# Kernel tuning notes

Hardware: AMD Instinct MI355X
Metric: run time of the kernel (lower is better)

Reference implementation:

```python
import jax, jax.numpy as jnp
import numpy as np

D_MODEL = 256
D_INNER = 512      # expand(2) * d_model
D_STATE = 16
DT_RANK = 16       # ceil(256/16)
D_CONV = 4
DEPTH = 2


def _silu(x):
    return x * jax.nn.sigmoid(x)


def _selective_scan(u, dt, A, B, C, D):
    # u,dt: [b,l,d]; A: [d,n]; B,C: [b,l,n]; D: [d]
    dA = jnp.einsum('bld,dn->bldn', dt, A)
    dBu = jnp.einsum('bld,bld,bln->bldn', dt, u, B)
    # torch: F.pad(dA[:,1:], last-l-dim one zero).flip(1).cumsum(1).exp().flip(1)
    dA_shift = jnp.concatenate([dA[:, 1:], jnp.zeros_like(dA[:, :1])], axis=1)
    dAc = jnp.exp(jnp.cumsum(dA_shift[:, ::-1], axis=1)[:, ::-1])
    x = jnp.cumsum(dBu * dAc, axis=1) / (dAc + 1e-12)
    y = jnp.einsum('bldn,bln->bld', x, C)
    return y + u * D


def _block(x, p):
    # x: [b,l,d_model]
    in_w, conv_w, conv_b, xproj_w, dt_w, dt_b, A_log, Dp, out_w = p
    xr = jnp.einsum('bld,ed->ble', x, in_w)           # [b,l,2*d_inner]
    xx, res = jnp.split(xr, 2, axis=-1)
    # causal depthwise conv1d (padding d_conv-1 then truncate == left-pad)
    xc = jax.lax.conv_general_dilated(
        xx.transpose(0, 2, 1), conv_w, window_strides=(1,),
        padding=[(D_CONV - 1, 0)], feature_group_count=D_INNER,
        dimension_numbers=('NCH', 'OIH', 'NCH')) + conv_b[None, :, None]
    xx = _silu(xc.transpose(0, 2, 1))                 # [b,l,d_inner]
    x_dbl = jnp.einsum('bld,ed->ble', xx, xproj_w)
    delta = x_dbl[..., :DT_RANK]
    B = x_dbl[..., DT_RANK:DT_RANK + D_STATE]
    C = x_dbl[..., DT_RANK + D_STATE:]
    delta = jax.nn.softplus(jnp.einsum('blr,dr->bld', delta, dt_w) + dt_b)
    A = -jnp.exp(A_log)
    y = _selective_scan(xx, delta, A, B, C, Dp)
    y = y * _silu(res)
    return jnp.einsum('bld,od->blo', y, out_w)


def _model1(x, params):
    for i in range(DEPTH):
        x = _block(x, tuple(q[i] for q in params))
    return x


def setup_inputs() -> dict:
    key = jax.random.key(0)
    ks = jax.random.split(key, 8)

    def nrm(k, shape, scale):
        return (jax.random.normal(k, shape) * scale).astype(jnp.float32)

    x0 = jax.random.normal(ks[0], (4, D_MODEL, 256, 256), jnp.float32)
    in_w = nrm(ks[1], (DEPTH, 2 * D_INNER, D_MODEL), 0.02)
    conv_w = nrm(ks[2], (DEPTH, D_INNER, 1, D_CONV), 0.1)
    conv_b = jnp.zeros((DEPTH, D_INNER), jnp.float32)
    xproj_w = nrm(ks[3], (DEPTH, DT_RANK + 2 * D_STATE, D_INNER), 0.02)
    dt_w = nrm(ks[4], (DEPTH, D_INNER, DT_RANK), 0.05)
    dt_b = jnp.full((DEPTH, D_INNER), -4.0, jnp.float32)  # small deltas for stability
    A_log = jnp.tile(jnp.log(jnp.arange(1, D_STATE + 1, dtype=jnp.float32))[None, None, :],
                     (DEPTH, D_INNER, 1))
    Dp = jnp.ones((DEPTH, D_INNER), jnp.float32)
    out_w = nrm(ks[5], (DEPTH, D_MODEL, D_INNER), 0.02)
    return dict(x0=x0, in_w=in_w, conv_w=conv_w, conv_b=conv_b, xproj_w=xproj_w,
                dt_w=dt_w, dt_b=dt_b, A_log=A_log, Dp=Dp, out_w=out_w)


def reference(x0, in_w, conv_w, conv_b, xproj_w, dt_w, dt_b, A_log, Dp, out_w):
    params = (in_w, conv_w, conv_b, xproj_w, dt_w, dt_b, A_log, Dp, out_w)
    # h-axis: pool over w, mamba over length h (weights shared with w pass)
    x_h = x0.mean(axis=3)                                        # [b,c,h]
    xm_h = _model1(x_h.transpose(0, 2, 1), params)               # [b,h,c]
    xm_h = xm_h.transpose(0, 2, 1)[..., None] * x0               # [b,c,h,w]
    # w-axis: pool over h of gated map, mamba over length w
    x_w = xm_h.mean(axis=2)                                      # [b,c,w]
    xm_w = _model1(x_w.transpose(0, 2, 1), params)               # [b,w,c]
    return xm_w.transpose(0, 2, 1)[:, :, None, :] * x0           # [b,c,h,w]
```

## Files before the change

kernel.cpp:

```cpp
#include <hip/hip_runtime.h>
#include <math.h>

#define BSZ 4
#define DM 256
#define LL 256
#define DI 512
#define NBL (BSZ * LL)

__device__ __forceinline__ float fast_rcp(float x) { return __builtin_amdgcn_rcpf(x); }
__device__ __forceinline__ float fast_sig(float x) { return fast_rcp(1.0f + __expf(-x)); }

__device__ __forceinline__ void unswz(int j, int& b, int& i) {
    b = (j & 7) >> 1;
    i = ((j >> 3) << 1) | (j & 1);
}

__global__ __launch_bounds__(256) void k_meanw_prep(const float* __restrict__ x0,
                                                    const float* __restrict__ in_w1,
                                                    const float* __restrict__ out_w0,
                                                    float* __restrict__ S0,
                                                    float* __restrict__ Wf) {
    __shared__ float smem[1664];
    int bl = blockIdx.x;
    int tid = threadIdx.x;
    if (bl < 1024) {
        int b, i; unswz(bl, b, i);
        int rowblk = (b << 8) | i;
        int wv = tid >> 6, lane = tid & 63;
        const float4* x4 = (const float4*)x0;
        int rbase = rowblk * 256 + wv * 64;
        for (int i0 = 0; i0 < 64; i0 += 8) {
            float s[8];
#pragma unroll
            for (int j = 0; j < 8; ++j) {
                float4 v = x4[(size_t)(rbase + i0 + j) * 64 + lane];
                s[j] = (v.x + v.y) + (v.z + v.w);
            }
#pragma unroll
            for (int j = 0; j < 8; ++j) {
#pragma unroll
                for (int m = 32; m >= 1; m >>= 1) s[j] += __shfl_xor(s[j], m);
            }
            if (lane == 0) {
#pragma unroll
                for (int j = 0; j < 8; ++j) {
                    int rr = rbase + i0 + j;
                    int bb = rr >> 16, d = (rr >> 8) & 255, h = rr & 255;
                    S0[((size_t)(bb * LL) + h) * DM + d] = s[j] * (1.0f / 256.0f);
                }
            }
        }
    } else {
        float* As = smem;
        float* Bs = smem + 576;
        int t = bl - 1024;
        int e0 = (t >> 4) * 32, k0c = (t & 15) * 32;
        int tx = tid & 15, ty = tid >> 4;
        float acc00 = 0.f, acc01 = 0.f, acc10 = 0.f, acc11 = 0.f;
        for (int dm0 = 0; dm0 < 256; dm0 += 16) {
            float4 v;
            if (tid < 128) {
                int r = tid >> 2, q = tid & 3;
                v = *(const float4*)(in_w1 + (size_t)(e0 + r) * 256 + dm0 + 4 * q);
            } else {
                int idx = tid - 128;
                int r = idx >> 3, q = idx & 7;
                v = *(const float4*)(out_w0 + (size_t)(dm0 + r) * 512 + k0c + 4 * q);
            }
            __syncthreads();
            if (tid < 128) {
                int r = tid >> 2, q = tid & 3;
                As[(4 * q + 0) * 36 + r] = v.x;
                As[(4 * q + 1) * 36 + r] = v.y;
                As[(4 * q + 2) * 36 + r] = v.z;
                As[(4 * q + 3) * 36 + r] = v.w;
            } else {
                int idx = tid - 128;
                int r = idx >> 3, q = idx & 7;
                Bs[r * 36 + 4 * q + 0] = v.x;
                Bs[r * 36 + 4 * q + 1] = v.y;
                Bs[r * 36 + 4 * q + 2] = v.z;
                Bs[r * 36 + 4 * q + 3] = v.w;
            }
            __syncthreads();
#pragma unroll
            for (int kk = 0; kk < 16; ++kk) {
                float2 a = *(const float2*)(As + kk * 36 + 2 * ty);
                float2 b2 = *(const float2*)(Bs + kk * 36 + 2 * tx);
                acc00 = fmaf(a.x, b2.x, acc00);
                acc01 = fmaf(a.x, b2.y, acc01);
                acc10 = fmaf(a.y, b2.x, acc10);
                acc11 = fmaf(a.y, b2.y, acc11);
            }
        }
        float* c0 = Wf + (size_t)(e0 + 2 * ty) * 512 + k0c + 2 * tx;
        c0[0] = acc00; c0[1] = acc01;
        c0[512] = acc10; c0[513] = acc11;
    }
}

__global__ __launch_bounds__(256) void k_gemm_nt64(const float* __restrict__ A,
                                                   const float* __restrict__ Bw,
                                                   float* __restrict__ C) {
    __shared__ float As[16][68];
    __shared__ float Bs[16][68];
    int tid = threadIdx.x;
    int b, i; unswz(blockIdx.x, b, i);
    int m0 = b * 256 + (i >> 4) * 64;
    int n0 = (i & 15) * 64;
    int tx = tid & 15, ty = tid >> 4;
    int r = tid >> 2, kq = (tid & 3) * 4;

    const float* pa = A + (size_t)(m0 + r) * 256 + kq;
    const float* pb = Bw + (size_t)(n0 + r) * 256 + kq;
    float4 ra = *(const float4*)pa;
    float4 rb = *(const float4*)pb;

    float acc[4][4];
#pragma unroll
    for (int ii = 0; ii < 4; ++ii)
#pragma unroll
        for (int jj = 0; jj < 4; ++jj) acc[ii][jj] = 0.0f;

    for (int k0 = 0; k0 < 256; k0 += 16) {
        __syncthreads();
        As[kq + 0][r] = ra.x; As[kq + 1][r] = ra.y; As[kq + 2][r] = ra.z; As[kq + 3][r] = ra.w;
        Bs[kq + 0][r] = rb.x; Bs[kq + 1][r] = rb.y; Bs[kq + 2][r] = rb.z; Bs[kq + 3][r] = rb.w;
        __syncthreads();
        if (k0 + 16 < 256) {
            ra = *(const float4*)(pa + k0 + 16);
            rb = *(const float4*)(pb + k0 + 16);
        }
#pragma unroll
        for (int kk = 0; kk < 16; ++kk) {
            float4 a4 = *(const float4*)(&As[kk][ty * 4]);
            float4 b4 = *(const float4*)(&Bs[kk][tx * 4]);
            float aa[4] = {a4.x, a4.y, a4.z, a4.w};
            float bb[4] = {b4.x, b4.y, b4.z, b4.w};
#pragma unroll
            for (int ii = 0; ii < 4; ++ii)
#pragma unroll
                for (int jj = 0; jj < 4; ++jj)
                    acc[ii][jj] = fmaf(aa[ii], bb[jj], acc[ii][jj]);
        }
    }
#pragma unroll
    for (int ii = 0; ii < 4; ++ii) {
        float4 o;
        o.x = acc[ii][0]; o.y = acc[ii][1]; o.z = acc[ii][2]; o.w = acc[ii][3];
        *(float4*)(C + (size_t)(m0 + ty * 4 + ii) * 1024 + n0 + tx * 4) = o;
    }
}

__global__ __launch_bounds__(256) void k_gemm_tn64(const float* __restrict__ At,
                                                   const float* __restrict__ Bw,
                                                   float* __restrict__ C) {
    __shared__ float As[16][68];
    __shared__ float Bs[16][68];
    int tid = threadIdx.x;
    int b, i; unswz(blockIdx.x, b, i);
    int l0 = (i >> 4) * 64;
    int n0 = (i & 15) * 64;
    int m0 = b * 256 + l0;
    int tx = tid & 15, ty = tid >> 4;
    int rkk = tid >> 4, mq = (tid & 15) * 4;
    int rn = tid >> 2, dq = (tid & 3) * 4;

    const float* pa = At + ((size_t)(b * 512) + rkk) * 256 + l0 + mq;
    const float* pb = Bw + (size_t)(n0 + rn) * 512 + dq;
    float4 ra = *(const float4*)pa;
    float4 rb = *(const float4*)pb;

    float acc[4][4];
#pragma unroll
    for (int ii = 0; ii < 4; ++ii)
#pragma unroll
        for (int jj = 0; jj < 4; ++jj) acc[ii][jj] = 0.0f;

    for (int d0 = 0; d0 < 512; d0 += 16) {
        __syncthreads();
        *(float4*)(&As[rkk][mq]) = ra;
        Bs[dq + 0][rn] = rb.x; Bs[dq + 1][rn] = rb.y; Bs[dq + 2][rn] = rb.z; Bs[dq + 3][rn] = rb.w;
        __syncthreads();
        if (d0 + 16 < 512) {
            ra = *(const float4*)(pa + (size_t)(d0 + 16) * 256);
            rb = *(const float4*)(pb + d0 + 16);
        }
#pragma unroll
        for (int kk = 0; kk < 16; ++kk) {
            float4 a4 = *(const float4*)(&As[kk][ty * 4]);
            float4 b4 = *(const float4*)(&Bs[kk][tx * 4]);
            float aa[4] = {a4.x, a4.y, a4.z, a4.w};
            float bb[4] = {b4.x, b4.y, b4.z, b4.w};
#pragma unroll
            for (int ii = 0; ii < 4; ++ii)
#pragma unroll
                for (int jj = 0; jj < 4; ++jj)
                    acc[ii][jj] = fmaf(aa[ii], bb[jj], acc[ii][jj]);
        }
    }
#pragma unroll
    for (int ii = 0; ii < 4; ++ii) {
        float4 o;
        o.x = acc[ii][0]; o.y = acc[ii][1]; o.z = acc[ii][2]; o.w = acc[ii][3];
        *(float4*)(C + (size_t)(m0 + ty * 4 + ii) * 1024 + n0 + tx * 4) = o;
    }
}

__global__ __launch_bounds__(256) void k_gemm_tn32(const float* __restrict__ At,
                                                   const float* __restrict__ B,
                                                   float* __restrict__ C) {
    __shared__ float As[16 * 36];
    __shared__ float Bs[16 * 36];
    int tid = threadIdx.x;
    int tx = tid & 15, ty = tid >> 4;
    int b, i; unswz(blockIdx.x, b, i);
    int l0 = (i >> 3) * 32;
    int n0 = (i & 7) * 32;
    int m0 = b * 256 + l0;

    float acc00 = 0.f, acc01 = 0.f, acc10 = 0.f, acc11 = 0.f;
    for (int d0 = 0; d0 < 512; d0 += 16) {
        float4 v;
        if (tid < 128) {
            int r = tid >> 3, q = tid & 7;
            v = *(const float4*)(At + ((size_t)(b * 512 + d0 + r)) * 256 + l0 + 4 * q);
        } else {
            int idx = tid - 128;
            int nr = idx >> 2, q = idx & 3;
            v = *(const float4*)(B + (size_t)(n0 + nr) * 512 + d0 + 4 * q);
        }
        __syncthreads();
        if (tid < 128) {
            int r = tid >> 3, q = tid & 7;
            *(float4*)(As + r * 36 + 4 * q) = v;
        } else {
            int idx = tid - 128;
            int nr = idx >> 2, q = idx & 3;
            Bs[(4 * q + 0) * 36 + nr] = v.x;
            Bs[(4 * q + 1) * 36 + nr] = v.y;
            Bs[(4 * q + 2) * 36 + nr] = v.z;
            Bs[(4 * q + 3) * 36 + nr] = v.w;
        }
        __syncthreads();
#pragma unroll
        for (int kk = 0; kk < 16; ++kk) {
            float2 a = *(const float2*)(As + kk * 36 + 2 * ty);
            float2 bb = *(const float2*)(Bs + kk * 36 + 2 * tx);
            acc00 = fmaf(a.x, bb.x, acc00);
            acc01 = fmaf(a.x, bb.y, acc01);
            acc10 = fmaf(a.y, bb.x, acc10);
            acc11 = fmaf(a.y, bb.y, acc11);
        }
    }
    float2 o0; o0.x = acc00; o0.y = acc01;
    float2 o1; o1.x = acc10; o1.y = acc11;
    *(float2*)(C + (size_t)(m0 + 2 * ty + 0) * 256 + n0 + 2 * tx) = o0;
    *(float2*)(C + (size_t)(m0 + 2 * ty + 1) * 256 + n0 + 2 * tx) = o1;
}

__global__ __launch_bounds__(256) void k_mid(const float* __restrict__ xz,
                                             const float* __restrict__ cw,
                                             const float* __restrict__ cb,
                                             const float* __restrict__ xpw,
                                             float* __restrict__ xx,
                                             float* __restrict__ xdbl) {
    __shared__ float xs[DI];
    __shared__ float pr[256];
    int tid = threadIdx.x;
    int b = (blockIdx.x & 7) >> 1;
    int ib = ((blockIdx.x >> 3) << 1) | (blockIdx.x & 1);

    for (int k = 0; k < 4; ++k) {
        int l = ib + 64 * k;
        int bl = (b << 8) | l;
        __syncthreads();
#pragma unroll
        for (int c = 0; c < 2; ++c) {
            int d = tid + 256 * c;
            float4 w4 = *(const float4*)(cw + d * 4);
            float acc = cb[d];
#pragma unroll
            for (int kk = 0; kk < 4; ++kk) {
                int ls = l + kk - 3;
                float v = (ls >= 0) ? xz[((size_t)(b * LL + ls)) * 1024 + d] : 0.0f;
                acc = fmaf(((const float*)&w4)[kk], v, acc);
            }
            float v = acc * fast_sig(acc);
            xs[d] = v;
            xx[(size_t)bl * DI + d] = v;
        }
        __syncthreads();

        int e = tid >> 2, c2 = tid & 3;
        float a = 0.0f;
        if (e < 48) {
            const float4* xv4 = (const float4*)(xs + c2 * 128);
            const float4* wv4 = (const float4*)(xpw + (size_t)e * DI + c2 * 128);
#pragma unroll 8
            for (int q = 0; q < 32; ++q) {
                float4 x4 = xv4[q], p4 = wv4[q];
                a = fmaf(x4.x, p4.x, a);
                a = fmaf(x4.y, p4.y, a);
                a = fmaf(x4.z, p4.z, a);
                a = fmaf(x4.w, p4.w, a);
            }
        }
        pr[tid] = a;
        __syncthreads();
        if (tid < 48)
            xdbl[(size_t)bl * 48 + tid] = pr[4 * tid] + pr[4 * tid + 1] + pr[4 * tid + 2] + pr[4 * tid + 3];
    }
}

__global__ __launch_bounds__(256) void k_scan(const float* __restrict__ xx,
                                              const float* __restrict__ xdbl,
                                              const float* __restrict__ xz,
                                              const float* __restrict__ Alog,
                                              const float* __restrict__ Dp,
                                              const float* __restrict__ dtw,
                                              const float* __restrict__ dtb,
                                              float* __restrict__ ygT) {
    __shared__ float yred[4][LL];
    __shared__ float us[LL];
    int tid = threadIdx.x;
    int lane = tid & 63, w = tid >> 6;
    int b = (blockIdx.x & 7) >> 1;
    int ib = ((blockIdx.x >> 3) << 1) | (blockIdx.x & 1);
    int l0 = lane * 4;

    for (int kq = 0; kq < 4; ++kq) {
        int d = ib + 128 * kq;
        int seq = b * DI + d;
        __syncthreads();

        const float* xd0 = xdbl + ((size_t)(b * LL) + l0) * 48;
        const float* wr = dtw + d * 16;
        float4 w0 = *(const float4*)(wr + 0);
        float4 w1 = *(const float4*)(wr + 4);
        float4 w2 = *(const float4*)(wr + 8);
        float4 w3 = *(const float4*)(wr + 12);
        float bias = dtb[d];

        float dt[4], u[4], dtu[4], P[4];
#pragma unroll
        for (int i = 0; i < 4; ++i) {
            const float* xr = xd0 + i * 48;
            float4 a0 = *(const float4*)(xr + 0);
            float4 a1 = *(const float4*)(xr + 4);
            float4 a2 = *(const float4*)(xr + 8);
            float4 a3 = *(const float4*)(xr + 12);
            float acc = bias;
            acc = fmaf(a0.x, w0.x, acc); acc = fmaf(a0.y, w0.y, acc);
            acc = fmaf(a0.z, w0.z, acc); acc = fmaf(a0.w, w0.w, acc);
            acc = fmaf(a1.x, w1.x, acc); acc = fmaf(a1.y, w1.y, acc);
            acc = fmaf(a1.z, w1.z, acc); acc = fmaf(a1.w, w1.w, acc);
            acc = fmaf(a2.x, w2.x, acc); acc = fmaf(a2.y, w2.y, acc);
            acc = fmaf(a2.z, w2.z, acc); acc = fmaf(a2.w, w2.w, acc);
            acc = fmaf(a3.x, w3.x, acc); acc = fmaf(a3.y, w3.y, acc);
            acc = fmaf(a3.z, w3.z, acc); acc = fmaf(a3.w, w3.w, acc);
            dt[i] = (acc > 20.0f) ? acc : __logf(1.0f + __expf(acc));
            u[i] = xx[((size_t)(b * LL) + l0 + i) * DI + d];
            dtu[i] = dt[i] * u[i];
        }

        P[0] = dt[0]; P[1] = P[0] + dt[1]; P[2] = P[1] + dt[2]; P[3] = P[2] + dt[3];
        float s = P[3];
#pragma unroll
        for (int off = 1; off < 64; off <<= 1) {
            float t = __shfl_up(s, off);
            if (lane >= off) s += t;
        }
        float base = s - P[3];
        float dt_end = __shfl(s, 63);
        float Dtc[4];
#pragma unroll
        for (int i = 0; i < 4; ++i) Dtc[i] = P[i] + base;

        if (w == 0) {
#pragma unroll
            for (int i = 0; i < 4; ++i) us[l0 + i] = u[i];
        }

        float4 Al = *(const float4*)(Alog + d * 16 + 4 * w);
        float A[4] = {-__expf(Al.x), -__expf(Al.y), -__expf(Al.z), -__expf(Al.w)};
        float Bv[4][4], Cv[4][4];
#pragma unroll
        for (int i = 0; i < 4; ++i) {
            float4 bq = *(const float4*)(xd0 + i * 48 + 16 + 4 * w);
            float4 cq = *(const float4*)(xd0 + i * 48 + 32 + 4 * w);
            Bv[i][0] = bq.x; Bv[i][1] = bq.y; Bv[i][2] = bq.z; Bv[i][3] = bq.w;
            Cv[i][0] = cq.x; Cv[i][1] = cq.y; Cv[i][2] = cq.z; Cv[i][3] = cq.w;
        }

        float y[4] = {0.f, 0.f, 0.f, 0.f};
#pragma unroll
        for (int c = 0; c < 4; ++c) {
            float Ac = A[c];
            float dAc[4], t[4];
#pragma unroll
            for (int i = 0; i < 4; ++i) {
                dAc[i] = __expf(Ac * (dt_end - Dtc[i]));
                t[i] = dtu[i] * Bv[i][c] * dAc[i];
            }
            float p0 = t[0], p1 = p0 + t[1], p2 = p1 + t[2], p3 = p2 + t[3];
            float ss = p3;
#pragma unroll
            for (int off = 1; off < 64; off <<= 1) {
                float tt = __shfl_up(ss, off);
                if (lane >= off) ss += tt;
            }
            float baseT = ss - p3;
            y[0] = fmaf((p0 + baseT) * fast_rcp(dAc[0] + 1e-12f), Cv[0][c], y[0]);
            y[1] = fmaf((p1 + baseT) * fast_rcp(dAc[1] + 1e-12f), Cv[1][c], y[1]);
            y[2] = fmaf((p2 + baseT) * fast_rcp(dAc[2] + 1e-12f), Cv[2][c], y[2]);
            y[3] = fmaf((p3 + baseT) * fast_rcp(dAc[3] + 1e-12f), Cv[3][c], y[3]);
        }
#pragma unroll
        for (int i = 0; i < 4; ++i) yred[w][l0 + i] = y[i];
        __syncthreads();

        int l = tid;
        float ysum = yred[0][l] + yred[1][l] + yred[2][l] + yred[3][l];
        float yv = fmaf(us[l], Dp[d], ysum);
        float res = xz[((size_t)(b * LL) + l) * 1024 + DI + d];
        ygT[(size_t)seq * LL + l] = yv * res * fast_sig(res);
    }
}

__global__ __launch_bounds__(256) void k_fuse_mean_h(const float* __restrict__ m,
                                                     const float* __restrict__ x0,
                                                     float* __restrict__ xw) {
    int b, d; unswz(blockIdx.x, b, d);
    int bd = (b << 8) | d;
    int w = threadIdx.x;
    __shared__ float ms[LL];
    ms[w] = m[((size_t)(b * LL) + w) * DM + d];
    __syncthreads();
    const float* xrow = x0 + (size_t)bd * 65536;
    float a0 = 0.0f, a1 = 0.0f, a2 = 0.0f, a3 = 0.0f;
    for (int h = 0; h < 256; h += 8) {
        float xv[8];
#pragma unroll
        for (int j = 0; j < 8; ++j) xv[j] = xrow[(size_t)(h + j) * 256 + w];
        a0 = fmaf(ms[h + 0], xv[0], a0);
        a1 = fmaf(ms[h + 1], xv[1], a1);
        a2 = fmaf(ms[h + 2], xv[2], a2);
        a3 = fmaf(ms[h + 3], xv[3], a3);
        a0 = fmaf(ms[h + 4], xv[4], a0);
        a1 = fmaf(ms[h + 5], xv[5], a1);
        a2 = fmaf(ms[h + 6], xv[6], a2);
        a3 = fmaf(ms[h + 7], xv[7], a3);
    }
    float acc = (a0 + a1) + (a2 + a3);
    xw[((size_t)(b * LL) + w) * DM + d] = acc * (1.0f / 256.0f);
}

__global__ __launch_bounds__(256) void k_final(const float* __restrict__ mw,
                                               const float* __restrict__ x0,
                                               float* __restrict__ out) {
    __shared__ float ms[LL];
    int b, d; unswz(blockIdx.x, b, d);
    int bd = (b << 8) | d;
    int tid = threadIdx.x;
    ms[tid] = mw[((size_t)(b * LL) + tid) * DM + d];
    __syncthreads();

    int w4 = tid & 63;
    int hq = tid >> 6;
    float4 mv = *(const float4*)(ms + (w4 << 2));
    const float4* xin = (const float4*)(x0 + (size_t)bd * 65536);
    float4* oout = (float4*)(out + (size_t)bd * 65536);
#pragma unroll 4
    for (int hi = 0; hi < 64; ++hi) {
        int h = hi * 4 + hq;
        size_t idx = (size_t)h * 64 + w4;
        float4 xv = xin[idx];
        float4 o;
        o.x = mv.x * xv.x;
        o.y = mv.y * xv.y;
        o.z = mv.z * xv.z;
        o.w = mv.w * xv.w;
        oout[idx] = o;
    }
}

extern "C" void kernel_launch(void* const* d_in, const int* in_sizes, int n_in,
                              void* d_out, int out_size, void* d_ws, size_t ws_size,
                              hipStream_t stream) {
    const float* x0      = (const float*)d_in[0];
    const float* in_w    = (const float*)d_in[1];
    const float* conv_w  = (const float*)d_in[2];
    const float* conv_b  = (const float*)d_in[3];
    const float* xproj_w = (const float*)d_in[4];
    const float* dt_w    = (const float*)d_in[5];
    const float* dt_b    = (const float*)d_in[6];
    const float* A_log   = (const float*)d_in[7];
    const float* Dp      = (const float*)d_in[8];
    const float* out_w   = (const float*)d_in[9];
    float* out = (float*)d_out;

    float* S0   = (float*)d_ws;
    float* Sout = S0 + 262144;
    float* Wf   = Sout + 262144;
    float* xz   = Wf + 524288;
    float* xx   = xz + 1048576;
    float* xdbl = xx + 524288;
    float* ygT  = xdbl + 49152;

    const float* out_w1 = out_w + 131072;

    auto run_model = [&](const float* inb, float* outb) {
        k_gemm_nt64<<<256, 256, 0, stream>>>(inb, in_w, xz);
        k_mid<<<256, 256, 0, stream>>>(xz, conv_w, conv_b, xproj_w, xx, xdbl);
        k_scan<<<512, 256, 0, stream>>>(xx, xdbl, xz, A_log, Dp, dt_w, dt_b, ygT);
        k_gemm_tn64<<<256, 256, 0, stream>>>(ygT, Wf, xz);
        k_mid<<<256, 256, 0, stream>>>(xz, conv_w + 2048, conv_b + 512,
                                       xproj_w + 24576, xx, xdbl);
        k_scan<<<512, 256, 0, stream>>>(xx, xdbl, xz, A_log + 8192, Dp + 512,
                                        dt_w + 8192, dt_b + 512, ygT);
        k_gemm_tn32<<<256, 256, 0, stream>>>(ygT, out_w1, outb);
    };

    k_meanw_prep<<<1536, 256, 0, stream>>>(x0, in_w + 262144, out_w, S0, Wf);
    run_model(S0, Sout);
    k_fuse_mean_h<<<NBL, 256, 0, stream>>>(Sout, x0, S0);
    run_model(S0, Sout);
    k_final<<<NBL, 256, 0, stream>>>(Sout, x0, out);
}
```

Before: 479.0 us.

## Fuse final out-projection GEMM into the mean-h and final gating kernels

Removes the standalone out-projection GEMM kernel. Each (b,d) block of the downstream gating kernels now computes its own column of the out-projection, a dot over 512 inner channels for all 256 positions, before doing the x0 pass. This saves two launches and the round trip of the intermediate Sout buffer. In exchange, each block reads a 512x256 slab of ygT, which makes the ygT traffic redundant across the 256 d-blocks that share a batch, though much of it should hit in cache.

```diff
diff --git a/kernel.cpp b/kernel.cpp
--- a/kernel.cpp
+++ b/kernel.cpp
@@ -205,58 +205,6 @@
         o.x = acc[ii][0]; o.y = acc[ii][1]; o.z = acc[ii][2]; o.w = acc[ii][3];
         *(float4*)(C + (size_t)(m0 + ty * 4 + ii) * 1024 + n0 + tx * 4) = o;
     }
-}
-
-__global__ __launch_bounds__(256) void k_gemm_tn32(const float* __restrict__ At,
-                                                   const float* __restrict__ B,
-                                                   float* __restrict__ C) {
-    __shared__ float As[16 * 36];
-    __shared__ float Bs[16 * 36];
-    int tid = threadIdx.x;
-    int tx = tid & 15, ty = tid >> 4;
-    int b, i; unswz(blockIdx.x, b, i);
-    int l0 = (i >> 3) * 32;
-    int n0 = (i & 7) * 32;
-    int m0 = b * 256 + l0;
-
-    float acc00 = 0.f, acc01 = 0.f, acc10 = 0.f, acc11 = 0.f;
-    for (int d0 = 0; d0 < 512; d0 += 16) {
-        float4 v;
-        if (tid < 128) {
-            int r = tid >> 3, q = tid & 7;
-            v = *(const float4*)(At + ((size_t)(b * 512 + d0 + r)) * 256 + l0 + 4 * q);
-        } else {
-            int idx = tid - 128;
-            int nr = idx >> 2, q = idx & 3;
-            v = *(const float4*)(B + (size_t)(n0 + nr) * 512 + d0 + 4 * q);
-        }
-        __syncthreads();
-        if (tid < 128) {
-            int r = tid >> 3, q = tid & 7;
-            *(float4*)(As + r * 36 + 4 * q) = v;
-        } else {
-            int idx = tid - 128;
-            int nr = idx >> 2, q = idx & 3;
-            Bs[(4 * q + 0) * 36 + nr] = v.x;
-            Bs[(4 * q + 1) * 36 + nr] = v.y;
-            Bs[(4 * q + 2) * 36 + nr] = v.z;
-            Bs[(4 * q + 3) * 36 + nr] = v.w;
-        }
-        __syncthreads();
-#pragma unroll
-        for (int kk = 0; kk < 16; ++kk) {
-            float2 a = *(const float2*)(As + kk * 36 + 2 * ty);
-            float2 bb = *(const float2*)(Bs + kk * 36 + 2 * tx);
-            acc00 = fmaf(a.x, bb.x, acc00);
-            acc01 = fmaf(a.x, bb.y, acc01);
-            acc10 = fmaf(a.y, bb.x, acc10);
-            acc11 = fmaf(a.y, bb.y, acc11);
-        }
-    }
-    float2 o0; o0.x = acc00; o0.y = acc01;
-    float2 o1; o1.x = acc10; o1.y = acc11;
-    *(float2*)(C + (size_t)(m0 + 2 * ty + 0) * 256 + n0 + 2 * tx) = o0;
-    *(float2*)(C + (size_t)(m0 + 2 * ty + 1) * 256 + n0 + 2 * tx) = o1;
 }
 
 __global__ __launch_bounds__(256) void k_mid(const float* __restrict__ xz,
@@ -428,15 +376,46 @@
     }
 }
 
-__global__ __launch_bounds__(256) void k_fuse_mean_h(const float* __restrict__ m,
-                                                     const float* __restrict__ x0,
-                                                     float* __restrict__ xw) {
+__device__ __forceinline__ void outproj_col(const float* __restrict__ ygT,
+                                            const float* __restrict__ w1row,
+                                            int b, int tid,
+                                            float* ws, float* ms) {
+    ws[tid] = w1row[tid];
+    ws[tid + 256] = w1row[tid + 256];
+    __syncthreads();
+    const float* yb = ygT + (size_t)(b * 512) * 256 + tid;
+    float a0 = 0.f, a1 = 0.f, a2 = 0.f, a3 = 0.f;
+#pragma unroll 2
+    for (int dd = 0; dd < 512; dd += 8) {
+        float v0 = yb[(dd + 0) * 256], v1 = yb[(dd + 1) * 256];
+        float v2 = yb[(dd + 2) * 256], v3 = yb[(dd + 3) * 256];
+        float v4 = yb[(dd + 4) * 256], v5 = yb[(dd + 5) * 256];
+        float v6 = yb[(dd + 6) * 256], v7 = yb[(dd + 7) * 256];
+        a0 = fmaf(v0, ws[dd + 0], a0);
+        a1 = fmaf(v1, ws[dd + 1], a1);
+        a2 = fmaf(v2, ws[dd + 2], a2);
+        a3 = fmaf(v3, ws[dd + 3], a3);
+        a0 = fmaf(v4, ws[dd + 4], a0);
+        a1 = fmaf(v5, ws[dd + 5], a1);
+        a2 = fmaf(v6, ws[dd + 6], a2);
+        a3 = fmaf(v7, ws[dd + 7], a3);
+    }
+    ms[tid] = (a0 + a1) + (a2 + a3);
+    __syncthreads();
+}
+
+__global__ __launch_bounds__(256) void k_outproj_fuse_mean_h(const float* __restrict__ ygT,
+                                                             const float* __restrict__ w1,
+                                                             const float* __restrict__ x0,
+                                                             float* __restrict__ xw) {
+    __shared__ float ws[512];
+    __shared__ float ms[LL];
     int b, d; unswz(blockIdx.x, b, d);
     int bd = (b << 8) | d;
-    int w = threadIdx.x;
-    __shared__ float ms[LL];
-    ms[w] = m[((size_t)(b * LL) + w) * DM + d];
-    __syncthreads();
+    int tid = threadIdx.x;
+    outproj_col(ygT, w1 + (size_t)d * 512, b, tid, ws, ms);
+
+    int w = tid;
     const float* xrow = x0 + (size_t)bd * 65536;
     float a0 = 0.0f, a1 = 0.0f, a2 = 0.0f, a3 = 0.0f;
     for (int h = 0; h < 256; h += 8) {
@@ -456,15 +435,16 @@
     xw[((size_t)(b * LL) + w) * DM + d] = acc * (1.0f / 256.0f);
 }
 
-__global__ __launch_bounds__(256) void k_final(const float* __restrict__ mw,
-                                               const float* __restrict__ x0,
-                                               float* __restrict__ out) {
+__global__ __launch_bounds__(256) void k_outproj_final(const float* __restrict__ ygT,
+                                                       const float* __restrict__ w1,
+                                                       const float* __restrict__ x0,
+                                                       float* __restrict__ out) {
+    __shared__ float ws[512];
     __shared__ float ms[LL];
     int b, d; unswz(blockIdx.x, b, d);
     int bd = (b << 8) | d;
     int tid = threadIdx.x;
-    ms[tid] = mw[((size_t)(b * LL) + tid) * DM + d];
-    __syncthreads();
+    outproj_col(ygT, w1 + (size_t)d * 512, b, tid, ws, ms);
 
     int w4 = tid & 63;
     int hq = tid >> 6;
@@ -501,8 +481,7 @@
     float* out = (float*)d_out;
 
     float* S0   = (float*)d_ws;
-    float* Sout = S0 + 262144;
-    float* Wf   = Sout + 262144;
+    float* Wf   = S0 + 262144;
     float* xz   = Wf + 524288;
     float* xx   = xz + 1048576;
     float* xdbl = xx + 524288;
@@ -510,7 +489,7 @@
 
     const float* out_w1 = out_w + 131072;
 
-    auto run_model = [&](const float* inb, float* outb) {
+    auto run_model_core = [&](const float* inb) {
         k_gemm_nt64<<<256, 256, 0, stream>>>(inb, in_w, xz);
         k_mid<<<256, 256, 0, stream>>>(xz, conv_w, conv_b, xproj_w, xx, xdbl);
         k_scan<<<512, 256, 0, stream>>>(xx, xdbl, xz, A_log, Dp, dt_w, dt_b, ygT);
@@ -519,12 +498,11 @@
                                        xproj_w + 24576, xx, xdbl);
         k_scan<<<512, 256, 0, stream>>>(xx, xdbl, xz, A_log + 8192, Dp + 512,
                                         dt_w + 8192, dt_b + 512, ygT);
-        k_gemm_tn32<<<256, 256, 0, stream>>>(ygT, out_w1, outb);
     };
 
     k_meanw_prep<<<1536, 256, 0, stream>>>(x0, in_w + 262144, out_w, S0, Wf);
-    run_model(S0, Sout);
-    k_fuse_mean_h<<<NBL, 256, 0, stream>>>(Sout, x0, S0);
-    run_model(S0, Sout);
-    k_final<<<NBL, 256, 0, stream>>>(Sout, x0, out);
-}
+    run_model_core(S0);
+    k_outproj_fuse_mean_h<<<NBL, 256, 0, stream>>>(ygT, out_w1, x0, S0);
+    run_model_core(S0);
+    k_outproj_final<<<NBL, 256, 0, stream>>>(ygT, out_w1, x0, out);
+}
```

After: 472.7 us. About the same (-1.3%).
